# Kernel tuning notes

Measured on AMD Instinct MI355X. Metric: run time of the kernel, lower is better.

## Reference

```python
import jax, jax.numpy as jnp
import numpy as np

DECAY = 0.6
THRESH = 0.6
MASK_T = 784 * 4  # default T in create_general_mask


def _make_mask(dim, c_min=10, c_max=50, min_dc=0.95, max_dc=0.99, T=MASK_T):
    # Faithful numpy port of create_general_mask (phase_shift_max=0.0 -> no shift).
    dcs = np.linspace(min_dc, max_dc, dim)
    cycles = np.linspace(c_min, c_max, dim)
    rows = []
    for cyc, dc in zip(cycles, dcs):
        cyc = int(np.ceil(cyc))
        on = int(np.ceil(dc * cyc))
        pat = [1] * on + [0] * (cyc - on)
        full = pat * (T // cyc) + pat[: T % cyc]
        rows.append(full)
    return jnp.asarray(np.array(rows, dtype=np.float32))  # [dim, T]


def setup_inputs() -> dict:
    key = jax.random.key(0)
    k1, k2, k3, k4, k5 = jax.random.split(key, 5)
    T, B, NTOKEN, NINP, H1, H2 = 128, 32, 32000, 256, 512, 512
    raw_input = jax.random.randint(k1, (T, B), 0, NTOKEN)
    enc_w = jax.random.uniform(k2, (NTOKEN, NINP), jnp.float32, -0.1, 0.1)
    # kaiming_uniform-like init: bound = sqrt(6 / fan_in), torch fan_in = dim 1
    b1 = float(np.sqrt(6.0 / H1))
    b2 = float(np.sqrt(6.0 / H2))
    fc1 = jax.random.uniform(k3, (NINP, H1), jnp.float32, -b1, b1)
    fc2 = jax.random.uniform(k4, (H1, H2), jnp.float32, -b2, b2)
    dec_w = jax.random.uniform(k5, (NTOKEN, H2), jnp.float32, -0.1, 0.1)
    dec_b = jnp.zeros((NTOKEN,), jnp.float32)
    mask1 = _make_mask(H1)
    mask2 = _make_mask(H2)
    return {"raw_input": raw_input, "enc_w": enc_w, "fc1": fc1, "fc2": fc2,
            "dec_w": dec_w, "dec_b": dec_b, "mask1": mask1, "mask2": mask2}


def _act(x):
    # ActFun.forward: heaviside spike
    return (x > 0.0).astype(x.dtype)


def reference(raw_input, enc_w, fc1, fc2, dec_w, dec_b, mask1, mask2):
    T, B = raw_input.shape
    emb = enc_w[raw_input]                    # [T, B, ninp] (dropout p=0 -> identity)
    m1 = mask1[:, :T].T                       # [T, H1]
    m2 = mask2[:, :T].T                       # [T, H2]

    def rhythm_update(fc, x, mem, m):
        state = x @ fc                        # [B, H]
        reset = (mem > THRESH).astype(x.dtype)
        new_mem = mem * (1.0 - reset) * DECAY + state
        mem = jnp.where(m == 0.0, mem, new_mem)   # mask broadcasts [H] -> [B, H]
        spike = _act(mem - THRESH) * m
        return mem, spike

    h1 = jnp.zeros((B, fc1.shape[1]), emb.dtype)
    h2 = jnp.zeros((B, fc2.shape[1]), emb.dtype)

    def step(carry, xs):
        h1m, h2m = carry
        x, ma, mb = xs
        h1m, s1 = rhythm_update(fc1, x, h1m, ma)
        h2m, s2 = rhythm_update(fc2, s1, h2m, mb)
        return (h1m, h2m), s2

    _, spikes = jax.lax.scan(step, (h1, h2), (emb, m1, m2))  # [T, B, H2]
    decoded = spikes @ dec_w.T + dec_b        # [T, B, ntoken]
    return decoded
```

## Files before the change

kernel.cpp:

```cpp
#include <hip/hip_runtime.h>


typedef __attribute__((ext_vector_type(8)))  short short8;
typedef __attribute__((ext_vector_type(16))) float f32x16;
typedef __attribute__((ext_vector_type(8)))  unsigned short us8;

#define WAITVM(N) asm volatile("s_waitcnt vmcnt(" #N ")" ::: "memory")
#define LGKM0()   asm volatile("s_waitcnt lgkmcnt(0)" ::: "memory")

__device__ __forceinline__ unsigned short f2bf(float f) {
    unsigned int u = __float_as_uint(f);
    unsigned int r = (u + 0x7FFFu + ((u >> 16) & 1u)) >> 16;
    return (unsigned short)r;
}

__global__ __launch_bounds__(256) void maskT_kernel(
    const float* __restrict__ m1, const float* __restrict__ m2,
    float* __restrict__ t1, float* __restrict__ t2)
{
    int i = blockIdx.x * 256 + threadIdx.x;
    int h = i >> 7, t = i & 127;
    t1[t * 512 + h] = m1[(size_t)h * 3136 + t];
    t2[t * 512 + h] = m2[(size_t)h * 3136 + t];
}

__global__ __launch_bounds__(256) void split_kernel(
    const float* __restrict__ w, unsigned short* __restrict__ w2, int n4)
{
    int i = blockIdx.x * 256 + threadIdx.x;
    if (i >= n4) return;
    float4 v = ((const float4*)w)[i];
    float vv[4] = {v.x, v.y, v.z, v.w};
    us8 o;
    #pragma unroll
    for (int c = 0; c < 4; ++c) {
        unsigned short hb = f2bf(vv[c]);
        float hf = __uint_as_float(((unsigned int)hb) << 16);
        o[2 * c]     = hb;
        o[2 * c + 1] = f2bf(vv[c] - hf);
    }
    ((us8*)w2)[i] = o;
}

__global__ __launch_bounds__(256) void gemm_f32_kernel(
    const float* __restrict__ A, const float* __restrict__ B,
    float* __restrict__ C, int M, int N, int K,
    const int* __restrict__ gidx, const float* __restrict__ gtable)
{
    __shared__ float As[32][132];
    __shared__ float Bs[32][68];
    int tid = threadIdx.x;
    int bn0 = blockIdx.x * 64, bm0 = blockIdx.y * 128;
    int ty = tid >> 4, tx = tid & 15;

    int arL  = tid >> 1;
    int akh  = (tid & 1) * 16;
    const float* Abase;
    size_t aoff;
    {
        int grow = bm0 + arL;
        if (gidx) { Abase = gtable; aoff = (size_t)gidx[grow] * K; }
        else      { Abase = A;      aoff = (size_t)grow * K; }
    }

    float acc[8][4];
    #pragma unroll
    for (int i = 0; i < 8; ++i)
        #pragma unroll
        for (int j = 0; j < 4; ++j) acc[i][j] = 0.f;

    for (int k0 = 0; k0 < K; k0 += 32) {
        float4 a4[4];
        #pragma unroll
        for (int i = 0; i < 4; ++i)
            a4[i] = *(const float4*)(Abase + aoff + k0 + akh + i * 4);
        float4 b4[2];
        #pragma unroll
        for (int i = 0; i < 2; ++i) {
            int f = tid + 256 * i;
            b4[i] = *(const float4*)(B + (size_t)(k0 + (f >> 4)) * N + bn0 + (f & 15) * 4);
        }
        __syncthreads();
        #pragma unroll
        for (int i = 0; i < 4; ++i) {
            As[akh + i * 4 + 0][arL] = a4[i].x;
            As[akh + i * 4 + 1][arL] = a4[i].y;
            As[akh + i * 4 + 2][arL] = a4[i].z;
            As[akh + i * 4 + 3][arL] = a4[i].w;
        }
        #pragma unroll
        for (int i = 0; i < 2; ++i) {
            int f = tid + 256 * i;
            *(float4*)&Bs[f >> 4][(f & 15) * 4] = b4[i];
        }
        __syncthreads();
        #pragma unroll
        for (int kk = 0; kk < 32; ++kk) {
            float a8[8];
            *(float4*)&a8[0] = *(const float4*)&As[kk][ty * 8];
            *(float4*)&a8[4] = *(const float4*)&As[kk][ty * 8 + 4];
            float4 bq = *(const float4*)&Bs[kk][tx * 4];
            float bb[4] = {bq.x, bq.y, bq.z, bq.w};
            #pragma unroll
            for (int i = 0; i < 8; ++i)
                #pragma unroll
                for (int j = 0; j < 4; ++j) acc[i][j] += a8[i] * bb[j];
        }
    }
    #pragma unroll
    for (int i = 0; i < 8; ++i) {
        float4 v = {acc[i][0], acc[i][1], acc[i][2], acc[i][3]};
        *(float4*)(C + (size_t)(bm0 + ty * 8 + i) * N + bn0 + tx * 4) = v;
    }
}

template <int DUP>
__global__ __launch_bounds__(64) void scan_kernel(
    const float* __restrict__ state, const float* __restrict__ maskT,
    float* __restrict__ outF, unsigned int* __restrict__ outU)
{
    int tid = blockIdx.x * 64 + threadIdx.x;
    int b = tid >> 9, h = tid & 511;
    float mem = 0.f;
    for (int t0 = 0; t0 < 128; t0 += 8) {
        float st8[8], m8[8];
        #pragma unroll
        for (int u = 0; u < 8; ++u) {
            st8[u] = state[(size_t)((t0 + u) * 32 + b) * 512 + h];
            m8[u]  = maskT[(t0 + u) * 512 + h];
        }
        #pragma unroll
        for (int u = 0; u < 8; ++u) {
            float nm = (mem > 0.6f) ? st8[u] : mem * 0.6f + st8[u];
            mem = (m8[u] == 0.0f) ? mem : nm;
            float spf = (mem > 0.6f) ? m8[u] : 0.0f;
            size_t ridx = (size_t)((t0 + u) * 32 + b) * 512 + h;
            if (DUP) outU[ridx] = f2bf(spf) * 0x10001u;
            else     outF[ridx] = spf;
        }
    }
}

__global__ __launch_bounds__(512, 2) void gemm3_kernel(
    const unsigned short* __restrict__ A,
    const unsigned short* __restrict__ W,
    const float* __restrict__ bias, float* __restrict__ C)
{
    constexpr int K = 1024, NTOK = 32000;
    __shared__ char lds[131072];

    int tid  = threadIdx.x;
    int lane = tid & 63;
    int wid  = __builtin_amdgcn_readfirstlane(tid >> 6);

    int bid = blockIdx.x;
    int swz = (bid & 7) * 250 + (bid >> 3);
    int mt = swz & 15;
    int nt = swz >> 4;
    int m0 = mt * 256, n0 = nt * 256;

    int wm = wid >> 2, wn = wid & 3;

    const unsigned short* srcB[4];
    int dstOff[4];
    #pragma unroll
    for (int i = 0; i < 4; ++i) {
        int q   = i * 512 + tid;
        int isB = q >> 10;
        int qq  = q & 1023;
        int j   = qq >> 3;
        int cp  = qq & 7;
        int c   = cp ^ (j & 7);
        int row = 2 * j + (c >> 2);
        srcB[i] = (isB ? W + (size_t)(n0 + row) * K
                       : A + (size_t)(m0 + row) * K) + (c & 3) * 8;
        dstOff[i] = (i * 512 + wid * 64) * 16;
    }

    int cl = lane & 31, hi5 = lane >> 5;
    int aOff[4], bOff[2];
    #pragma unroll
    for (int mi = 0; mi < 4; ++mi) {
        int R = wm * 128 + mi * 32 + cl;
        int j = R >> 1;
        int c = (hi5 + 4 * (R & 1)) ^ (j & 7);
        aOff[mi] = j * 128 + c * 16;
    }
    #pragma unroll
    for (int ni = 0; ni < 2; ++ni) {
        int R = wn * 64 + ni * 32 + cl;
        int j = R >> 1;
        int c = (hi5 + 4 * (R & 1)) ^ (j & 7);
        bOff[ni] = 16384 + j * 128 + c * 16;
    }

    f32x16 acc[4][2];
    #pragma unroll
    for (int i = 0; i < 4; ++i)
        #pragma unroll
        for (int j = 0; j < 2; ++j)
            #pragma unroll
            for (int e = 0; e < 16; ++e) acc[i][j][e] = 0.f;

    auto GLOAD = [&](int i, int kt) {
        __builtin_amdgcn_global_load_lds(
            (const __attribute__((address_space(1))) unsigned int*)(srcB[i] + kt * 32),
            (__attribute__((address_space(3))) unsigned int*)(lds + ((kt & 3) << 15) + dstOff[i]),
            16, 0, 0);
    };

    auto STEP = [&](int t, bool stage) {
        const char* base = lds + ((t & 3) << 15);
        #pragma unroll
        for (int ki = 0; ki < 2; ++ki) {
            if (stage) { GLOAD(2 * ki, t + 3); GLOAD(2 * ki + 1, t + 3); }
            short8 fa[4], fb[2];
            int kx = ki * 32;
            #pragma unroll
            for (int mi = 0; mi < 4; ++mi)
                fa[mi] = *(const short8*)(base + (aOff[mi] ^ kx));
            #pragma unroll
            for (int ni = 0; ni < 2; ++ni)
                fb[ni] = *(const short8*)(base + (bOff[ni] ^ kx));
            __builtin_amdgcn_s_barrier();
            LGKM0();
            __builtin_amdgcn_sched_barrier(0);
            __builtin_amdgcn_s_setprio(1);
            #pragma unroll
            for (int mi = 0; mi < 4; ++mi)
                #pragma unroll
                for (int ni = 0; ni < 2; ++ni)
                    acc[mi][ni] = __builtin_amdgcn_mfma_f32_32x32x16_bf16(
                        fa[mi], fb[ni], acc[mi][ni], 0, 0, 0);
            __builtin_amdgcn_s_setprio(0);
        }
    };

    #pragma unroll
    for (int kt = 0; kt < 3; ++kt)
        #pragma unroll
        for (int i = 0; i < 4; ++i) GLOAD(i, kt);
    WAITVM(8);
    __builtin_amdgcn_s_barrier();

    for (int t = 0; t < 29; ++t) {
        STEP(t, true);
        WAITVM(8);
        __builtin_amdgcn_s_barrier();
    }
    STEP(29, false);
    WAITVM(4);
    __builtin_amdgcn_s_barrier();
    STEP(30, false);
    WAITVM(0);
    __builtin_amdgcn_s_barrier();
    STEP(31, false);

    #pragma unroll
    for (int ni = 0; ni < 2; ++ni) {
        int gc = n0 + wn * 64 + ni * 32 + cl;
        float bv = bias[gc];
        #pragma unroll
        for (int mi = 0; mi < 4; ++mi) {
            f32x16 v = acc[mi][ni];
            #pragma unroll
            for (int reg = 0; reg < 16; ++reg) {
                int gr = m0 + wm * 128 + mi * 32 + (reg & 3) + 8 * (reg >> 2) + 4 * hi5;
                C[(size_t)gr * NTOK + gc] = v[reg] + bv;
            }
        }
    }
}

extern "C" void kernel_launch(void* const* d_in, const int* in_sizes, int n_in,
                              void* d_out, int out_size, void* d_ws, size_t ws_size,
                              hipStream_t stream)
{
    const int*   raw   = (const int*)  d_in[0];
    const float* enc_w = (const float*)d_in[1];
    const float* fc1   = (const float*)d_in[2];
    const float* fc2   = (const float*)d_in[3];
    const float* dec_w = (const float*)d_in[4];
    const float* dec_b = (const float*)d_in[5];
    const float* mask1 = (const float*)d_in[6];
    const float* mask2 = (const float*)d_in[7];
    float* out = (float*)d_out;

    const int H1 = 512, H2 = 512, NINP = 256, NTOK = 32000;
    const int M = 128 * 32;

    char* ws = (char*)d_ws;
    float*          st  = (float*)ws;
    float*          spF = (float*)(ws + (size_t)(8u << 20));
    unsigned int*   a2u = (unsigned int*)(ws + (size_t)(8u << 20));
    unsigned short* A2  = (unsigned short*)(ws + (size_t)(8u << 20));
    unsigned short* W2  = (unsigned short*)(ws + (size_t)(16u << 20));
    float* mT1 = (float*)d_out;
    float* mT2 = (float*)d_out + 65536;

    maskT_kernel<<<256, 256, 0, stream>>>(mask1, mask2, mT1, mT2);

    int n4 = NTOK * H2 / 4;
    split_kernel<<<(n4 + 255) / 256, 256, 0, stream>>>(dec_w, W2, n4);

    gemm_f32_kernel<<<dim3(H1 / 64, M / 128), 256, 0, stream>>>(
        nullptr, fc1, st, M, H1, NINP, raw, enc_w);

    scan_kernel<0><<<256, 64, 0, stream>>>(st, mT1, spF, nullptr);

    gemm_f32_kernel<<<dim3(H2 / 64, M / 128), 256, 0, stream>>>(
        spF, fc2, st, M, H2, H1, nullptr, nullptr);

    scan_kernel<1><<<256, 64, 0, stream>>>(st, mT2, nullptr, a2u);

    gemm3_kernel<<<(M / 256) * (NTOK / 256), 512, 0, stream>>>(A2, W2, dec_b, out);

    (void)in_sizes; (void)n_in; (void)out_size; (void)ws_size;
}
```

Measured before the change: 916.1 us.

## Retile decoder GEMM to 128x128 blocks with 16x16x32 MFMA

Shrinks the decoder GEMM block tile from 256x256 with 512 threads to 128x128 with 256 threads and halves LDS use. It also switches from 32x32x16 to 16x16x32 bf16 MFMA and splits each k-step into two MFMA phases around the async global-to-LDS loads. The aim is more blocks for better CU occupancy and a smaller tail wave. The cost is lower data reuse per block, more global traffic, and narrower 64-byte output store segments.

```diff
diff --git a/kernel.cpp b/kernel.cpp
--- a/kernel.cpp
+++ b/kernel.cpp
@@ -2,7 +2,7 @@
 
 
 typedef __attribute__((ext_vector_type(8)))  short short8;
-typedef __attribute__((ext_vector_type(16))) float f32x16;
+typedef __attribute__((ext_vector_type(4)))  float f32x4;
 typedef __attribute__((ext_vector_type(8)))  unsigned short us8;
 
 #define WAITVM(N) asm volatile("s_waitcnt vmcnt(" #N ")" ::: "memory")
@@ -141,99 +141,104 @@
     }
 }
 
-__global__ __launch_bounds__(512, 2) void gemm3_kernel(
+__global__ __launch_bounds__(256, 2) void gemm3_kernel(
     const unsigned short* __restrict__ A,
     const unsigned short* __restrict__ W,
     const float* __restrict__ bias, float* __restrict__ C)
 {
     constexpr int K = 1024, NTOK = 32000;
-    __shared__ char lds[131072];
+    __shared__ char lds[65536];
 
     int tid  = threadIdx.x;
     int lane = tid & 63;
     int wid  = __builtin_amdgcn_readfirstlane(tid >> 6);
 
     int bid = blockIdx.x;
-    int swz = (bid & 7) * 250 + (bid >> 3);
-    int mt = swz & 15;
-    int nt = swz >> 4;
-    int m0 = mt * 256, n0 = nt * 256;
-
-    int wm = wid >> 2, wn = wid & 3;
+    int swz = (bid & 7) * 1000 + (bid >> 3);
+    int mt = swz & 31;
+    int nt = swz >> 5;
+    int m0 = mt * 128, n0 = nt * 128;
+
+    int wm = wid >> 1, wn = wid & 1;
 
     const unsigned short* srcB[4];
     int dstOff[4];
     #pragma unroll
     for (int i = 0; i < 4; ++i) {
-        int q   = i * 512 + tid;
-        int isB = q >> 10;
-        int qq  = q & 1023;
+        int q   = i * 256 + tid;
+        int isB = q >> 9;
+        int qq  = q & 511;
         int j   = qq >> 3;
         int cp  = qq & 7;
         int c   = cp ^ (j & 7);
         int row = 2 * j + (c >> 2);
         srcB[i] = (isB ? W + (size_t)(n0 + row) * K
                        : A + (size_t)(m0 + row) * K) + (c & 3) * 8;
-        dstOff[i] = (i * 512 + wid * 64) * 16;
-    }
-
-    int cl = lane & 31, hi5 = lane >> 5;
-    int aOff[4], bOff[2];
-    #pragma unroll
-    for (int mi = 0; mi < 4; ++mi) {
-        int R = wm * 128 + mi * 32 + cl;
-        int j = R >> 1;
-        int c = (hi5 + 4 * (R & 1)) ^ (j & 7);
-        aOff[mi] = j * 128 + c * 16;
-    }
-    #pragma unroll
-    for (int ni = 0; ni < 2; ++ni) {
-        int R = wn * 64 + ni * 32 + cl;
-        int j = R >> 1;
-        int c = (hi5 + 4 * (R & 1)) ^ (j & 7);
-        bOff[ni] = 16384 + j * 128 + c * 16;
-    }
-
-    f32x16 acc[4][2];
+        dstOff[i] = (i * 256 + wid * 64) * 16;
+    }
+
+    int r = lane & 15, co = lane >> 4;
+    int aOff[4], bOff[4];
+    #pragma unroll
+    for (int mf = 0; mf < 4; ++mf) {
+        int row = wm * 64 + mf * 16 + r;
+        int j = row >> 1, c = co + 4 * (row & 1);
+        aOff[mf] = (j * 8 + (c ^ (j & 7))) * 16;
+    }
+    #pragma unroll
+    for (int nf = 0; nf < 4; ++nf) {
+        int row = wn * 64 + nf * 16 + r;
+        int j = row >> 1, c = co + 4 * (row & 1);
+        bOff[nf] = 8192 + (j * 8 + (c ^ (j & 7))) * 16;
+    }
+
+    f32x4 acc[4][4];
     #pragma unroll
     for (int i = 0; i < 4; ++i)
         #pragma unroll
-        for (int j = 0; j < 2; ++j)
-            #pragma unroll
-            for (int e = 0; e < 16; ++e) acc[i][j][e] = 0.f;
+        for (int j = 0; j < 4; ++j) acc[i][j] = (f32x4){0.f, 0.f, 0.f, 0.f};
 
     auto GLOAD = [&](int i, int kt) {
         __builtin_amdgcn_global_load_lds(
             (const __attribute__((address_space(1))) unsigned int*)(srcB[i] + kt * 32),
-            (__attribute__((address_space(3))) unsigned int*)(lds + ((kt & 3) << 15) + dstOff[i]),
+            (__attribute__((address_space(3))) unsigned int*)(lds + ((kt & 3) << 14) + dstOff[i]),
             16, 0, 0);
     };
 
     auto STEP = [&](int t, bool stage) {
-        const char* base = lds + ((t & 3) << 15);
-        #pragma unroll
-        for (int ki = 0; ki < 2; ++ki) {
-            if (stage) { GLOAD(2 * ki, t + 3); GLOAD(2 * ki + 1, t + 3); }
-            short8 fa[4], fb[2];
-            int kx = ki * 32;
+        const char* base = lds + ((t & 3) << 14);
+        short8 fa0[2], fb[4], fa1[2];
+        if (stage) { GLOAD(0, t + 3); GLOAD(1, t + 3); }
+        #pragma unroll
+        for (int f = 0; f < 2; ++f) fa0[f] = *(const short8*)(base + aOff[f]);
+        #pragma unroll
+        for (int f = 0; f < 4; ++f) fb[f]  = *(const short8*)(base + bOff[f]);
+        __builtin_amdgcn_s_barrier();
+        LGKM0();
+        __builtin_amdgcn_sched_barrier(0);
+        __builtin_amdgcn_s_setprio(1);
+        #pragma unroll
+        for (int mf = 0; mf < 2; ++mf)
             #pragma unroll
-            for (int mi = 0; mi < 4; ++mi)
-                fa[mi] = *(const short8*)(base + (aOff[mi] ^ kx));
+            for (int nf = 0; nf < 4; ++nf)
+                acc[mf][nf] = __builtin_amdgcn_mfma_f32_16x16x32_bf16(
+                    fa0[mf], fb[nf], acc[mf][nf], 0, 0, 0);
+        __builtin_amdgcn_s_setprio(0);
+        __builtin_amdgcn_s_barrier();
+        if (stage) { GLOAD(2, t + 3); GLOAD(3, t + 3); }
+        #pragma unroll
+        for (int f = 0; f < 2; ++f) fa1[f] = *(const short8*)(base + aOff[2 + f]);
+        __builtin_amdgcn_s_barrier();
+        LGKM0();
+        __builtin_amdgcn_sched_barrier(0);
+        __builtin_amdgcn_s_setprio(1);
+        #pragma unroll
+        for (int mf = 0; mf < 2; ++mf)
             #pragma unroll
-            for (int ni = 0; ni < 2; ++ni)
-                fb[ni] = *(const short8*)(base + (bOff[ni] ^ kx));
-            __builtin_amdgcn_s_barrier();
-            LGKM0();
-            __builtin_amdgcn_sched_barrier(0);
-            __builtin_amdgcn_s_setprio(1);
-            #pragma unroll
-            for (int mi = 0; mi < 4; ++mi)
-                #pragma unroll
-                for (int ni = 0; ni < 2; ++ni)
-                    acc[mi][ni] = __builtin_amdgcn_mfma_f32_32x32x16_bf16(
-                        fa[mi], fb[ni], acc[mi][ni], 0, 0, 0);
-            __builtin_amdgcn_s_setprio(0);
-        }
+            for (int nf = 0; nf < 4; ++nf)
+                acc[2 + mf][nf] = __builtin_amdgcn_mfma_f32_16x16x32_bf16(
+                    fa1[mf], fb[nf], acc[2 + mf][nf], 0, 0, 0);
+        __builtin_amdgcn_s_setprio(0);
     };
 
     #pragma unroll
@@ -256,18 +261,18 @@
     __builtin_amdgcn_s_barrier();
     STEP(31, false);
 
-    #pragma unroll
-    for (int ni = 0; ni < 2; ++ni) {
-        int gc = n0 + wn * 64 + ni * 32 + cl;
+    int lr = lane >> 4, lc = lane & 15;
+    #pragma unroll
+    for (int nf = 0; nf < 4; ++nf) {
+        int gc = n0 + wn * 64 + nf * 16 + lc;
         float bv = bias[gc];
         #pragma unroll
-        for (int mi = 0; mi < 4; ++mi) {
-            f32x16 v = acc[mi][ni];
+        for (int mf = 0; mf < 4; ++mf) {
+            int gr = m0 + wm * 64 + mf * 16 + lr * 4;
+            f32x4 v = acc[mf][nf];
             #pragma unroll
-            for (int reg = 0; reg < 16; ++reg) {
-                int gr = m0 + wm * 128 + mi * 32 + (reg & 3) + 8 * (reg >> 2) + 4 * hi5;
-                C[(size_t)gr * NTOK + gc] = v[reg] + bv;
-            }
+            for (int j = 0; j < 4; ++j)
+                C[(size_t)(gr + j) * NTOK + gc] = v[j] + bv;
         }
     }
 }
@@ -313,7 +318,7 @@
 
     scan_kernel<1><<<256, 64, 0, stream>>>(st, mT2, nullptr, a2u);
 
-    gemm3_kernel<<<(M / 256) * (NTOK / 256), 512, 0, stream>>>(A2, W2, dec_b, out);
+    gemm3_kernel<<<(M / 128) * (NTOK / 128), 256, 0, stream>>>(A2, W2, dec_b, out);
 
     (void)in_sizes; (void)n_in; (void)out_size; (void)ws_size;
 }
```

After: 1.035 ms. +12.9%, slower.
